# Optimization experiments

Measured on AMD Instinct MI355X. Metric: run time of the kernel, lower is better.

## Reference

```python
import jax, jax.numpy as jnp
import numpy as np

BSZ, QLEN, KLEN = 2, 1024, 2048
QD = KD = VD = HID = 1024
NH = 16
HD = HID // NH
SCALE = 1.0 / (HD ** 0.5)
NEG_INF = -1e30


def setup_inputs() -> dict:
    key = jax.random.key(0)
    ks = jax.random.split(key, 8)
    query = jax.random.normal(ks[0], (BSZ, QLEN, QD), dtype=jnp.float32)
    k_in = jax.random.normal(ks[1], (BSZ, KLEN, KD), dtype=jnp.float32)
    v_in = jax.random.normal(ks[2], (BSZ, KLEN, VD), dtype=jnp.float32)
    attn_mask = jax.random.randint(ks[3], (BSZ, KLEN), 0, 2, dtype=jnp.int32)
    # xavier_uniform for Linear(in, out) without bias; stored as [in, out]
    def xavier(k, fan_in, fan_out):
        lim = (6.0 / (fan_in + fan_out)) ** 0.5
        return jax.random.uniform(k, (fan_in, fan_out), jnp.float32, -lim, lim)
    Wq = xavier(ks[4], QD, HID)
    Wk = xavier(ks[5], KD, HID)
    Wv = xavier(ks[6], VD, HID)
    Wo = xavier(ks[7], HID, QD)
    return {"query": query, "key": k_in, "value": v_in, "attn_mask": attn_mask,
            "Wq": Wq, "Wk": Wk, "Wv": Wv, "Wo": Wo}


def reference(query, key, value, attn_mask, Wq, Wk, Wv, Wo):
    bsz, qlen, _ = query.shape
    klen = key.shape[1]
    # projections -> [b, len, n_head, head_dim]
    head_q = (query @ Wq).reshape(bsz, qlen, NH, HD)
    head_k = (key @ Wk).reshape(bsz, klen, NH, HD)
    head_v = (value @ Wv).reshape(bsz, klen, NH, HD)
    # attn scores [b, i, j, n]
    attn_score = jnp.einsum('bind,bjnd->bijn', head_q, head_k) * SCALE
    # 2D mask [b, j]: broadcast over query dim (axis 1) and head dim (axis 3)
    mask = (attn_mask == 0)[:, None, :, None]
    attn_score = jnp.where(mask, NEG_INF, attn_score)
    # configurable activation: sigmoid (no normalization over klen)
    attn_prob = jax.nn.sigmoid(attn_score)
    attn_vec = jnp.einsum('bijn,bjnd->bind', attn_prob, head_v)
    attn_vec = attn_vec.reshape(bsz, qlen, HID)
    return attn_vec @ Wo
```

## Files before the change

### kernel.cpp

```cpp
#include <hip/hip_runtime.h>
#include <hip/hip_bf16.h>

#define BSZ 2
#define QLEN 1024
#define KLEN 2048
#define HID 1024
#define NH 16
#define HD 64
#define SCALE 0.125f

using f32x4 = __attribute__((ext_vector_type(4))) float;
using bf16x8 = __attribute__((ext_vector_type(8))) short;
using u32x4 = __attribute__((ext_vector_type(4))) unsigned int;
using u32x2 = __attribute__((ext_vector_type(2))) unsigned int;
typedef unsigned short u16;

__device__ __forceinline__ u16 f2bf(float x) {
    unsigned int u = __builtin_bit_cast(unsigned int, x);
    u += 0x7FFFu + ((u >> 16) & 1u);
    return (u16)(u >> 16);
}
__device__ __forceinline__ unsigned int pack2bf(float a, float b) {
    return (unsigned int)f2bf(a) | ((unsigned int)f2bf(b) << 16);
}
__device__ __forceinline__ float sigm(float x) {
    return 1.0f / (1.0f + __expf(-x));
}
__device__ __forceinline__ f32x4 zero4() {
    f32x4 z = {0.0f, 0.0f, 0.0f, 0.0f};
    return z;
}

__device__ __forceinline__ void gl16(const void* g, void* l) {
    __builtin_amdgcn_global_load_lds(
        (const __attribute__((address_space(1))) void*)g,
        (__attribute__((address_space(3))) void*)l, 16, 0, 0);
}

template<int ROWS>
__device__ __forceinline__ void stage64(const u16* __restrict__ g, size_t gstride,
                                        u16* lds, int tid) {
    const int lane = tid & 63, wv = tid >> 6;
    constexpr int RPW = ROWS / 4;
#pragma unroll
    for (int c = 0; c < RPW / 8; ++c) {
        int row = wv * RPW + c * 8 + (lane >> 3);
        int cg = (lane & 7) ^ (row & 7);
        gl16(g + (size_t)row * gstride + cg * 8, lds + (size_t)(wv * RPW + c * 8) * 64);
    }
}

__global__ __launch_bounds__(256) void a2bf_kernel(
    const float* __restrict__ Aq, const float* __restrict__ Ak,
    const float* __restrict__ Av,
    u16* __restrict__ qbf, u16* __restrict__ kbf, u16* __restrict__ vbf)
{
    const int bid = blockIdx.x;
    const float* src; u16* dst; size_t base;
    if (bid < 1024)      { src = Aq; dst = qbf; base = (size_t)bid * 2048; }
    else if (bid < 3072) { src = Ak; dst = kbf; base = (size_t)(bid - 1024) * 2048; }
    else                 { src = Av; dst = vbf; base = (size_t)(bid - 3072) * 2048; }
    size_t e = base + (size_t)threadIdx.x * 8;
    float4 x0 = *(const float4*)&src[e];
    float4 x1 = *(const float4*)&src[e + 4];
    u32x4 w;
    w[0] = pack2bf(x0.x, x0.y); w[1] = pack2bf(x0.z, x0.w);
    w[2] = pack2bf(x1.x, x1.y); w[3] = pack2bf(x1.z, x1.w);
    *(u32x4*)&dst[e] = w;
}

__global__ __launch_bounds__(256) void wtrans_kernel(
    const float* __restrict__ W0, const float* __restrict__ W1,
    const float* __restrict__ W2, const float* __restrict__ W3,
    u16* __restrict__ T0, u16* __restrict__ T1,
    u16* __restrict__ T2, u16* __restrict__ T3)
{
    const float* W = blockIdx.z == 0 ? W0 : blockIdx.z == 1 ? W1 : blockIdx.z == 2 ? W2 : W3;
    u16* T = blockIdx.z == 0 ? T0 : blockIdx.z == 1 ? T1 : blockIdx.z == 2 ? T2 : T3;
    __shared__ float tile[64][65];
    const int tid = threadIdx.x;
    const int r0 = blockIdx.x * 64;
    const int c0 = blockIdx.y * 64;
#pragma unroll
    for (int i = 0; i < 4; ++i) {
        int ch = i * 256 + tid;
        int row = ch >> 4, cg = ch & 15;
        float4 x = *(const float4*)&W[(size_t)(r0 + row) * 1024 + c0 + cg * 4];
        tile[row][cg * 4 + 0] = x.x;
        tile[row][cg * 4 + 1] = x.y;
        tile[row][cg * 4 + 2] = x.z;
        tile[row][cg * 4 + 3] = x.w;
    }
    __syncthreads();
#pragma unroll
    for (int i = 0; i < 2; ++i) {
        int ch = i * 256 + tid;
        int orow = ch >> 3, ocg = ch & 7;
        u32x4 o;
#pragma unroll
        for (int j = 0; j < 4; ++j)
            o[j] = pack2bf(tile[ocg * 8 + 2 * j][orow], tile[ocg * 8 + 2 * j + 1][orow]);
        *(u32x4*)&T[(size_t)(c0 + orow) * 1024 + r0 + ocg * 8] = o;
    }
}

__global__ __launch_bounds__(256) void qkv_gemm_kernel(
    const u16* __restrict__ Aq, const u16* __restrict__ Ak, const u16* __restrict__ Av,
    const u16* __restrict__ Bq, const u16* __restrict__ Bk, const u16* __restrict__ Bv,
    u16* __restrict__ hq, u16* __restrict__ hk, u16* __restrict__ hvT)
{
    __shared__ u32x4 lds[2048];
    u16* As = (u16*)lds;
    u16* Bs = (u16*)(lds + 1024);

    const int i = blockIdx.x;
    const int bid = (i & 7) * 80 + (i >> 3);
    const u16* A; const u16* Bt; u16* C; int lb, task;
    if (bid < 128)      { task = 0; A = Aq; Bt = Bq; C = hq; lb = bid; }
    else if (bid < 384) { task = 1; A = Ak; Bt = Bk; C = hk; lb = bid - 128; }
    else                { task = 2; A = Av; Bt = Bv; C = nullptr; lb = bid - 384; }
    const int m0 = (lb >> 3) * 128, n0 = (lb & 7) * 128;

    const int tid = threadIdx.x;
    const int lane = tid & 63, wv = tid >> 6;
    const int wr = wv >> 1, wc = wv & 1;
    const int m = lane & 15, g = lane >> 4;

    f32x4 acc[4][4];
#pragma unroll
    for (int i2 = 0; i2 < 4; ++i2)
#pragma unroll
        for (int j = 0; j < 4; ++j) acc[i2][j] = zero4();

    for (int k0 = 0; k0 < 1024; k0 += 64) {
        stage64<128>(A  + (size_t)m0 * 1024 + k0, 1024, As, tid);
        stage64<128>(Bt + (size_t)n0 * 1024 + k0, 1024, Bs, tid);
        __syncthreads();
#pragma unroll
        for (int kk = 0; kk < 64; kk += 32) {
            bf16x8 af[4], bfr[4];
#pragma unroll
            for (int mi = 0; mi < 4; ++mi) {
                int row = wr * 64 + mi * 16 + m;
                af[mi] = *(const bf16x8*)&As[(row * 64 + kk + g * 8) ^ ((row & 7) << 3)];
            }
#pragma unroll
            for (int ni = 0; ni < 4; ++ni) {
                int row = wc * 64 + ni * 16 + m;
                bfr[ni] = *(const bf16x8*)&Bs[(row * 64 + kk + g * 8) ^ ((row & 7) << 3)];
            }
#pragma unroll
            for (int mi = 0; mi < 4; ++mi)
#pragma unroll
                for (int ni = 0; ni < 4; ++ni)
                    acc[mi][ni] = __builtin_amdgcn_mfma_f32_16x16x32_bf16(
                        af[mi], bfr[ni], acc[mi][ni], 0, 0, 0);
        }
        __syncthreads();
    }

    if (task < 2) {
#pragma unroll
        for (int mi = 0; mi < 4; ++mi)
#pragma unroll
            for (int r = 0; r < 4; ++r) {
                int row = m0 + wr * 64 + mi * 16 + g * 4 + r;
#pragma unroll
                for (int ni = 0; ni < 4; ++ni) {
                    int col = n0 + wc * 64 + ni * 16 + m;
                    C[(size_t)row * HID + col] = f2bf(acc[mi][ni][r]);
                }
            }
    } else {
        u16* T = (u16*)lds;
        __syncthreads();
#pragma unroll
        for (int mi = 0; mi < 4; ++mi)
#pragma unroll
            for (int ni = 0; ni < 4; ++ni)
#pragma unroll
                for (int r = 0; r < 4; ++r) {
                    int row = wr * 64 + mi * 16 + g * 4 + r;
                    int col = wc * 64 + ni * 16 + m;
                    T[col * 128 + ((((row >> 3) ^ (col & 7)) << 3) + (row & 7))] =
                        f2bf(acc[mi][ni][r]);
                }
        __syncthreads();
        const int b = m0 >> 11, kv0 = m0 & 2047;
#pragma unroll
        for (int it = 0; it < 8; ++it) {
            int idx = it * 256 + tid;
            int orow = idx >> 4, og = idx & 15;
            u32x4 x = *(const u32x4*)&T[orow * 128 + ((og ^ (orow & 7)) << 3)];
            *(u32x4*)&hvT[(size_t)(b * HID + n0 + orow) * KLEN + kv0 + og * 8] = x;
        }
    }
}

__global__ __launch_bounds__(256) void attn_kernel(
    const u16* __restrict__ hq, const u16* __restrict__ hk,
    const u16* __restrict__ hvT, const int* __restrict__ amask,
    float* __restrict__ O0, float* __restrict__ O1)
{
    __shared__ u32x4 KsBuf[512];
    __shared__ u32x4 VtBuf[512];
    __shared__ __align__(16) float Ml[64];
    __shared__ __align__(16) u16 Pw[4][16 * 40];
    u16* Ks = (u16*)KsBuf;
    u16* Vt = (u16*)VtBuf;

    const int tid = threadIdx.x;
    const int lane = tid & 63, wv = tid >> 6;
    const int m = lane & 15, g = lane >> 4;
    const int qt = blockIdx.x, h = blockIdx.y;
    const int b = blockIdx.z >> 1, sp = blockIdx.z & 1;
    const int qrow0 = qt * 64 + wv * 16;
    float* Op = sp ? O1 : O0;
    u16* P = Pw[wv];

    const u16* qp = &hq[(size_t)(b * QLEN + qrow0 + m) * HID + h * HD + g * 8];
    bf16x8 qf0 = *(const bf16x8*)qp;
    bf16x8 qf1 = *(const bf16x8*)(qp + 32);

    const u16* kbase = hk + (size_t)(b * KLEN + sp * 1024) * HID + h * HD;
    const u16* vbase = hvT + (size_t)(b * HID + h * HD) * KLEN + sp * 1024;
    const int* mbase = amask + b * KLEN + sp * 1024;

    f32x4 o[4];
#pragma unroll
    for (int i = 0; i < 4; ++i) o[i] = zero4();

    for (int kv0 = 0; kv0 < 1024; kv0 += 64) {
        stage64<64>(kbase + (size_t)kv0 * HID, HID, Ks, tid);
        stage64<64>(vbase + kv0, KLEN, Vt, tid);
        if (tid < 64) Ml[tid] = (mbase[kv0 + tid] != 0) ? 1.0f : 0.0f;
        __syncthreads();

#pragma unroll
        for (int sub = 0; sub < 2; ++sub) {
#pragma unroll
            for (int t = 0; t < 2; ++t) {
                int kvr = sub * 32 + t * 16 + m;
                bf16x8 ak0 = *(const bf16x8*)&Ks[(kvr * 64 + g * 8) ^ ((kvr & 7) << 3)];
                bf16x8 ak1 = *(const bf16x8*)&Ks[(kvr * 64 + 32 + g * 8) ^ ((kvr & 7) << 3)];
                f32x4 s = zero4();
                s = __builtin_amdgcn_mfma_f32_16x16x32_bf16(ak0, qf0, s, 0, 0, 0);
                s = __builtin_amdgcn_mfma_f32_16x16x32_bf16(ak1, qf1, s, 0, 0, 0);
                f32x4 mk = *(const f32x4*)&Ml[sub * 32 + t * 16 + 4 * g];
                float p0 = mk[0] * sigm(s[0] * SCALE);
                float p1 = mk[1] * sigm(s[1] * SCALE);
                float p2 = mk[2] * sigm(s[2] * SCALE);
                float p3 = mk[3] * sigm(s[3] * SCALE);
                u32x2 pp = { pack2bf(p0, p1), pack2bf(p2, p3) };
                *(u32x2*)&P[m * 40 + t * 16 + 4 * g] = pp;
            }
            bf16x8 pa = *(const bf16x8*)&P[m * 40 + 8 * g];
#pragma unroll
            for (int nt = 0; nt < 4; ++nt) {
                int d = 16 * nt + m;
                bf16x8 vt = *(const bf16x8*)&Vt[(d * 64 + sub * 32 + g * 8) ^ ((d & 7) << 3)];
                o[nt] = __builtin_amdgcn_mfma_f32_16x16x32_bf16(pa, vt, o[nt], 0, 0, 0);
            }
        }
        __syncthreads();
    }
#pragma unroll
    for (int nt = 0; nt < 4; ++nt)
#pragma unroll
        for (int r = 0; r < 4; ++r)
            Op[(size_t)(b * QLEN + qrow0 + 4 * g + r) * HID + h * HD + 16 * nt + m] =
                o[nt][r];
}

__global__ __launch_bounds__(256) void oproj_kernel(
    const float* __restrict__ O0, const float* __restrict__ O1,
    const u16* __restrict__ Bt, float* __restrict__ out)
{
    __shared__ u32x4 lds[1536];
    u16* As = (u16*)lds;
    u16* Bs = (u16*)(lds + 512);

    const int tid = threadIdx.x;
    const int lane = tid & 63, wv = tid >> 6;
    const int wr = wv >> 1, wc = wv & 1;
    const int m = lane & 15, g = lane >> 4;
    const int m0 = blockIdx.x * 64, n0 = blockIdx.y * 128;

    f32x4 acc[2][4];
#pragma unroll
    for (int i = 0; i < 2; ++i)
#pragma unroll
        for (int j = 0; j < 4; ++j) acc[i][j] = zero4();

    for (int k0 = 0; k0 < 1024; k0 += 64) {
        stage64<128>(Bt + (size_t)n0 * 1024 + k0, 1024, Bs, tid);
#pragma unroll
        for (int c = 0; c < 2; ++c) {
            int idx = c * 256 + tid;
            int row = idx >> 3, cg = idx & 7;
            size_t off = (size_t)(m0 + row) * 1024 + k0 + cg * 8;
            float4 a0 = *(const float4*)&O0[off];
            float4 a1 = *(const float4*)&O0[off + 4];
            float4 b0 = *(const float4*)&O1[off];
            float4 b1 = *(const float4*)&O1[off + 4];
            u32x4 w;
            w[0] = pack2bf(a0.x + b0.x, a0.y + b0.y);
            w[1] = pack2bf(a0.z + b0.z, a0.w + b0.w);
            w[2] = pack2bf(a1.x + b1.x, a1.y + b1.y);
            w[3] = pack2bf(a1.z + b1.z, a1.w + b1.w);
            *(u32x4*)&As[(row * 64 + cg * 8) ^ ((row & 7) << 3)] = w;
        }
        __syncthreads();
#pragma unroll
        for (int kk = 0; kk < 64; kk += 32) {
            bf16x8 af[2], bfr[4];
#pragma unroll
            for (int mi = 0; mi < 2; ++mi) {
                int row = wr * 32 + mi * 16 + m;
                af[mi] = *(const bf16x8*)&As[(row * 64 + kk + g * 8) ^ ((row & 7) << 3)];
            }
#pragma unroll
            for (int ni = 0; ni < 4; ++ni) {
                int row = wc * 64 + ni * 16 + m;
                bfr[ni] = *(const bf16x8*)&Bs[(row * 64 + kk + g * 8) ^ ((row & 7) << 3)];
            }
#pragma unroll
            for (int mi = 0; mi < 2; ++mi)
#pragma unroll
                for (int ni = 0; ni < 4; ++ni)
                    acc[mi][ni] = __builtin_amdgcn_mfma_f32_16x16x32_bf16(
                        af[mi], bfr[ni], acc[mi][ni], 0, 0, 0);
        }
        __syncthreads();
    }
#pragma unroll
    for (int mi = 0; mi < 2; ++mi)
#pragma unroll
        for (int r = 0; r < 4; ++r) {
            int row = m0 + wr * 32 + mi * 16 + g * 4 + r;
#pragma unroll
            for (int ni = 0; ni < 4; ++ni) {
                int col = n0 + wc * 64 + ni * 16 + m;
                out[(size_t)row * HID + col] = acc[mi][ni][r];
            }
        }
}

extern "C" void kernel_launch(void* const* d_in, const int* in_sizes, int n_in,
                              void* d_out, int out_size, void* d_ws, size_t ws_size,
                              hipStream_t stream)
{
    const float* query = (const float*)d_in[0];
    const float* key   = (const float*)d_in[1];
    const float* value = (const float*)d_in[2];
    const int*   amask = (const int*)d_in[3];
    const float* Wq    = (const float*)d_in[4];
    const float* Wk    = (const float*)d_in[5];
    const float* Wv    = (const float*)d_in[6];
    const float* Wo    = (const float*)d_in[7];

    char* ws = (char*)d_ws;
    u16* wtq = (u16*)(ws + (0ull  << 20));
    u16* wtk = (u16*)(ws + (2ull  << 20));
    u16* wtv = (u16*)(ws + (4ull  << 20));
    u16* wto = (u16*)(ws + (6ull  << 20));
    u16* hq  = (u16*)(ws + (8ull  << 20));
    u16* hk  = (u16*)(ws + (12ull << 20));
    u16* hvT = (u16*)(ws + (20ull << 20));
    u16* qbf = (u16*)(ws + (28ull << 20));
    u16* kbf = (u16*)(ws + (32ull << 20));
    u16* vbf = (u16*)(ws + (40ull << 20));
    float* O0 = (float*)(ws + (28ull << 20));
    float* O1 = (float*)(ws + (36ull << 20));

    a2bf_kernel<<<dim3(5120), 256, 0, stream>>>(query, key, value, qbf, kbf, vbf);
    wtrans_kernel<<<dim3(16, 16, 4), 256, 0, stream>>>(Wq, Wk, Wv, Wo, wtq, wtk, wtv, wto);
    qkv_gemm_kernel<<<dim3(640), 256, 0, stream>>>(qbf, kbf, vbf, wtq, wtk, wtv, hq, hk, hvT);
    attn_kernel<<<dim3(16, 16, 4), 256, 0, stream>>>(hq, hk, hvT, amask, O0, O1);
    oproj_kernel<<<dim3(32, 8), 256, 0, stream>>>(O0, O1, wto, (float*)d_out);
}
```

Baseline: 223.7 us.

## Double-buffer K/V tiles in attention, remap blocks, use hardware bf16 pack and rcp

The attention kernel now double-buffers the K, V and mask tiles in LDS, so the global-to-LDS loads for the next 64-row tile are issued while the current tile is computed. This is meant to hide load latency behind the MFMA and sigmoid work. The grid is flattened to 1D and block IDs are remapped so that adjacent blocks land on different XCDs. Float-to-bf16 conversion switches to the hardware v_cvt_pk_bf16_f32 instruction, and the sigmoid uses the fast rcp intrinsic; both trade a little rounding accuracy for fewer instructions. LDS use doubles, which could lower occupancy.

After: 202.0 us. 1.11x faster.

```diff
diff --git a/kernel.cpp b/kernel.cpp
--- a/kernel.cpp
+++ b/kernel.cpp
@@ -15,17 +15,13 @@
 using u32x2 = __attribute__((ext_vector_type(2))) unsigned int;
 typedef unsigned short u16;
 
-__device__ __forceinline__ u16 f2bf(float x) {
-    unsigned int u = __builtin_bit_cast(unsigned int, x);
-    u += 0x7FFFu + ((u >> 16) & 1u);
-    return (u16)(u >> 16);
-}
-__device__ __forceinline__ unsigned int pack2bf(float a, float b) {
-    return (unsigned int)f2bf(a) | ((unsigned int)f2bf(b) << 16);
-}
-__device__ __forceinline__ float sigm(float x) {
-    return 1.0f / (1.0f + __expf(-x));
-}
+__device__ __forceinline__ unsigned int cvtpk(float a, float b) {
+    unsigned int r;
+    asm("v_cvt_pk_bf16_f32 %0, %1, %2" : "=v"(r) : "v"(a), "v"(b));
+    return r;
+}
+__device__ __forceinline__ unsigned int pack2bf(float a, float b) { return cvtpk(a, b); }
+__device__ __forceinline__ u16 f2bf(float x) { return (u16)cvtpk(x, x); }
 __device__ __forceinline__ f32x4 zero4() {
     f32x4 z = {0.0f, 0.0f, 0.0f, 0.0f};
     return z;
@@ -197,26 +193,61 @@
     }
 }
 
+__device__ __forceinline__ void attn_tile(
+    const u16* __restrict__ Ks, const u16* __restrict__ Vt,
+    const float* __restrict__ Mlc, u16* __restrict__ P,
+    bf16x8 qf0, bf16x8 qf1, int m, int g, f32x4* o)
+{
+#pragma unroll
+    for (int sub = 0; sub < 2; ++sub) {
+#pragma unroll
+        for (int t = 0; t < 2; ++t) {
+            int kvr = sub * 32 + t * 16 + m;
+            bf16x8 ak0 = *(const bf16x8*)&Ks[(kvr * 64 + g * 8) ^ ((kvr & 7) << 3)];
+            bf16x8 ak1 = *(const bf16x8*)&Ks[(kvr * 64 + 32 + g * 8) ^ ((kvr & 7) << 3)];
+            f32x4 s = zero4();
+            s = __builtin_amdgcn_mfma_f32_16x16x32_bf16(ak0, qf0, s, 0, 0, 0);
+            s = __builtin_amdgcn_mfma_f32_16x16x32_bf16(ak1, qf1, s, 0, 0, 0);
+            f32x4 mk = *(const f32x4*)&Mlc[sub * 32 + t * 16 + 4 * g];
+            float p0 = mk[0] * __builtin_amdgcn_rcpf(1.0f + __expf(s[0] * -SCALE));
+            float p1 = mk[1] * __builtin_amdgcn_rcpf(1.0f + __expf(s[1] * -SCALE));
+            float p2 = mk[2] * __builtin_amdgcn_rcpf(1.0f + __expf(s[2] * -SCALE));
+            float p3 = mk[3] * __builtin_amdgcn_rcpf(1.0f + __expf(s[3] * -SCALE));
+            u32x2 pp = { cvtpk(p0, p1), cvtpk(p2, p3) };
+            *(u32x2*)&P[m * 40 + t * 16 + 4 * g] = pp;
+        }
+        bf16x8 pa = *(const bf16x8*)&P[m * 40 + 8 * g];
+#pragma unroll
+        for (int nt = 0; nt < 4; ++nt) {
+            int d = 16 * nt + m;
+            bf16x8 vt = *(const bf16x8*)&Vt[(d * 64 + sub * 32 + g * 8) ^ ((d & 7) << 3)];
+            o[nt] = __builtin_amdgcn_mfma_f32_16x16x32_bf16(pa, vt, o[nt], 0, 0, 0);
+        }
+    }
+}
+
 __global__ __launch_bounds__(256) void attn_kernel(
     const u16* __restrict__ hq, const u16* __restrict__ hk,
     const u16* __restrict__ hvT, const int* __restrict__ amask,
     float* __restrict__ O0, float* __restrict__ O1)
 {
-    __shared__ u32x4 KsBuf[512];
-    __shared__ u32x4 VtBuf[512];
-    __shared__ __align__(16) float Ml[64];
+    __shared__ u32x4 KsBuf[2][512];
+    __shared__ u32x4 VtBuf[2][512];
+    __shared__ __align__(16) float Ml[2][64];
     __shared__ __align__(16) u16 Pw[4][16 * 40];
-    u16* Ks = (u16*)KsBuf;
-    u16* Vt = (u16*)VtBuf;
 
     const int tid = threadIdx.x;
     const int lane = tid & 63, wv = tid >> 6;
     const int m = lane & 15, g = lane >> 4;
-    const int qt = blockIdx.x, h = blockIdx.y;
-    const int b = blockIdx.z >> 1, sp = blockIdx.z & 1;
+    const int li = blockIdx.x;
+    const int bid = (li & 7) * 128 + (li >> 3);
+    const int qt = bid & 15, h = (bid >> 4) & 15, z = bid >> 8;
+    const int b = z >> 1, sp = z & 1;
     const int qrow0 = qt * 64 + wv * 16;
     float* Op = sp ? O1 : O0;
     u16* P = Pw[wv];
+    u16* Ks0 = (u16*)KsBuf[0]; u16* Ks1 = (u16*)KsBuf[1];
+    u16* Vt0 = (u16*)VtBuf[0]; u16* Vt1 = (u16*)VtBuf[1];
 
     const u16* qp = &hq[(size_t)(b * QLEN + qrow0 + m) * HID + h * HD + g * 8];
     bf16x8 qf0 = *(const bf16x8*)qp;
@@ -230,38 +261,24 @@
 #pragma unroll
     for (int i = 0; i < 4; ++i) o[i] = zero4();
 
-    for (int kv0 = 0; kv0 < 1024; kv0 += 64) {
-        stage64<64>(kbase + (size_t)kv0 * HID, HID, Ks, tid);
-        stage64<64>(vbase + kv0, KLEN, Vt, tid);
-        if (tid < 64) Ml[tid] = (mbase[kv0 + tid] != 0) ? 1.0f : 0.0f;
-        __syncthreads();
-
-#pragma unroll
-        for (int sub = 0; sub < 2; ++sub) {
-#pragma unroll
-            for (int t = 0; t < 2; ++t) {
-                int kvr = sub * 32 + t * 16 + m;
-                bf16x8 ak0 = *(const bf16x8*)&Ks[(kvr * 64 + g * 8) ^ ((kvr & 7) << 3)];
-                bf16x8 ak1 = *(const bf16x8*)&Ks[(kvr * 64 + 32 + g * 8) ^ ((kvr & 7) << 3)];
-                f32x4 s = zero4();
-                s = __builtin_amdgcn_mfma_f32_16x16x32_bf16(ak0, qf0, s, 0, 0, 0);
-                s = __builtin_amdgcn_mfma_f32_16x16x32_bf16(ak1, qf1, s, 0, 0, 0);
-                f32x4 mk = *(const f32x4*)&Ml[sub * 32 + t * 16 + 4 * g];
-                float p0 = mk[0] * sigm(s[0] * SCALE);
-                float p1 = mk[1] * sigm(s[1] * SCALE);
-                float p2 = mk[2] * sigm(s[2] * SCALE);
-                float p3 = mk[3] * sigm(s[3] * SCALE);
-                u32x2 pp = { pack2bf(p0, p1), pack2bf(p2, p3) };
-                *(u32x2*)&P[m * 40 + t * 16 + 4 * g] = pp;
-            }
-            bf16x8 pa = *(const bf16x8*)&P[m * 40 + 8 * g];
-#pragma unroll
-            for (int nt = 0; nt < 4; ++nt) {
-                int d = 16 * nt + m;
-                bf16x8 vt = *(const bf16x8*)&Vt[(d * 64 + sub * 32 + g * 8) ^ ((d & 7) << 3)];
-                o[nt] = __builtin_amdgcn_mfma_f32_16x16x32_bf16(pa, vt, o[nt], 0, 0, 0);
-            }
-        }
+    stage64<64>(kbase, HID, Ks0, tid);
+    stage64<64>(vbase, KLEN, Vt0, tid);
+    if (tid < 64) Ml[0][tid] = (mbase[tid] != 0) ? 1.0f : 0.0f;
+    __syncthreads();
+
+#pragma unroll 1
+    for (int it = 0; it < 16; it += 2) {
+        stage64<64>(kbase + (size_t)(it + 1) * 64 * HID, HID, Ks1, tid);
+        stage64<64>(vbase + (it + 1) * 64, KLEN, Vt1, tid);
+        if (tid < 64) Ml[1][tid] = (mbase[(it + 1) * 64 + tid] != 0) ? 1.0f : 0.0f;
+        attn_tile(Ks0, Vt0, Ml[0], P, qf0, qf1, m, g, o);
+        __syncthreads();
+        if (it + 2 < 16) {
+            stage64<64>(kbase + (size_t)(it + 2) * 64 * HID, HID, Ks0, tid);
+            stage64<64>(vbase + (it + 2) * 64, KLEN, Vt0, tid);
+            if (tid < 64) Ml[0][tid] = (mbase[(it + 2) * 64 + tid] != 0) ? 1.0f : 0.0f;
+        }
+        attn_tile(Ks1, Vt1, Ml[1], P, qf0, qf1, m, g, o);
         __syncthreads();
     }
 #pragma unroll
@@ -376,6 +393,6 @@
     a2bf_kernel<<<dim3(5120), 256, 0, stream>>>(query, key, value, qbf, kbf, vbf);
     wtrans_kernel<<<dim3(16, 16, 4), 256, 0, stream>>>(Wq, Wk, Wv, Wo, wtq, wtk, wtv, wto);
     qkv_gemm_kernel<<<dim3(640), 256, 0, stream>>>(qbf, kbf, vbf, wtq, wtk, wtv, hq, hk, hvT);
-    attn_kernel<<<dim3(16, 16, 4), 256, 0, stream>>>(hq, hk, hvT, amask, O0, O1);
+    attn_kernel<<<dim3(1024), 256, 0, stream>>>(hq, hk, hvT, amask, O0, O1);
     oproj_kernel<<<dim3(32, 8), 256, 0, stream>>>(O0, O1, wto, (float*)d_out);
 }
```
